# Optimization experiments

Hardware: AMD Instinct MI355X
Metric: run time of the kernel (lower is better)

Reference implementation:

```python
import jax, jax.numpy as jnp
import numpy as np

KEYS = ["A1", "B2", "E1", "E2", "E3", "E4", "E5"]
DIMS = [1, 1, 2, 2, 2, 2, 2]  # irrep dimensions for D12 point group
H = 8  # num_heads


def setup_inputs() -> dict:
    key = jax.random.key(0)
    ks = jax.random.split(key, 11)
    B, S, M = 8, 1024, 64  # batch, seq_len, multiplicity per key
    inp = {}
    for i, (name, d) in enumerate(zip(KEYS, DIMS)):
        inp[f"x_{name}"] = jax.random.normal(ks[i], (B, S, d, M), dtype=jnp.float32)
    for j, wn in enumerate(["Wq", "Wk", "Wv", "Wo"]):
        # per-key nn.Linear weights [out_mult, in_mult], stacked over the 7 keys
        inp[wn] = jax.random.normal(ks[7 + j], (7, M, M), dtype=jnp.float32) / np.float32(np.sqrt(M))
    return inp


def _split_heads(v):
    # [B,S,d,m] -> [B,H,S,d*mk]
    B, S, d, m = v.shape
    mk = m // H
    return v.reshape(B, S, d, H, mk).transpose(0, 3, 1, 2, 4).reshape(B, H, S, d * mk)


def _combine_heads(v, d):
    # [B,H,S,d*mk] -> [B,S,d,H*mk]
    B, _, S, dmk = v.shape
    mk = dmk // d
    return v.reshape(B, H, S, d, mk).transpose(0, 2, 3, 1, 4).reshape(B, S, d, H * mk)


def _forward(xs, Wq, Wk, Wv, Wo):
    # per-key bias-free linears on the multiplicity (last) axis; nn.Linear does x @ W.T
    qs = [_split_heads(jnp.einsum('bsdi,oi->bsdo', x, Wq[i])) for i, x in enumerate(xs)]
    kks = [_split_heads(jnp.einsum('bsdi,oi->bsdo', x, Wk[i])) for i, x in enumerate(xs)]
    vs = [_split_heads(jnp.einsum('bsdi,oi->bsdo', x, Wv[i])) for i, x in enumerate(xs)]
    Q = jnp.concatenate(qs, axis=-1)  # [B,H,S,D], D = sum d_k*mk = 96
    K = jnp.concatenate(kks, axis=-1)
    scale = np.float32(1.0 / np.sqrt(Q.shape[-1]))
    probs = jax.nn.softmax(jnp.einsum('bhqd,bhkd->bhqk', Q, K) * scale, axis=-1)
    outs = []
    for i, (v, d) in enumerate(zip(vs, DIMS)):
        o = jnp.einsum('bhqk,bhkd->bhqd', probs, v)  # shared softmax over per-key V branches
        o = _combine_heads(o, d)  # [B,S,d,M]
        outs.append(jnp.einsum('bsdi,oi->bsdo', o, Wo[i]))
    # concatenate the 7 per-key outputs along the irrep-dimension axis: [B,S,12,M]
    return jnp.concatenate(outs, axis=2)


def reference(x_A1, x_B2, x_E1, x_E2, x_E3, x_E4, x_E5, Wq, Wk, Wv, Wo):
    xs = [x_A1, x_B2, x_E1, x_E2, x_E3, x_E4, x_E5]
    return _forward(xs, Wq, Wk, Wv, Wo)
```

## Files before the change

kernel.cpp:

```cpp
#include <hip/hip_runtime.h>
#include <stdint.h>

typedef __attribute__((ext_vector_type(8))) short bf16x8;
typedef __attribute__((ext_vector_type(4))) float f32x4;
typedef unsigned short ushort_t;

__device__ __forceinline__ unsigned short f2bf(float f){
  union { float f; unsigned u; } c; c.f = f;
  unsigned u = c.u;
  u = u + 0x7FFFu + ((u >> 16) & 1u);
  return (unsigned short)(u >> 16);
}

__device__ __forceinline__ bf16x8 cvt8(const float* p){
  const float4 a = ((const float4*)p)[0];
  const float4 b = ((const float4*)p)[1];
  bf16x8 r;
  r[0]=(short)f2bf(a.x); r[1]=(short)f2bf(a.y); r[2]=(short)f2bf(a.z); r[3]=(short)f2bf(a.w);
  r[4]=(short)f2bf(b.x); r[5]=(short)f2bf(b.y); r[6]=(short)f2bf(b.z); r[7]=(short)f2bf(b.w);
  return r;
}

__device__ __forceinline__ uint32_t pk2bf(float a, float b){
  uint32_t r;
  asm("v_cvt_pk_bf16_f32 %0, %1, %2" : "=v"(r) : "v"(a), "v"(b));
  return r;
}

__device__ __forceinline__ float exp2x(float x){
  float r;
  asm("v_exp_f32 %0, %1" : "=v"(r) : "v"(x));
  return r;
}

__device__ __forceinline__ void gll16(const ushort_t* g, short* l){
  __builtin_amdgcn_global_load_lds(
      (const __attribute__((address_space(1))) unsigned int*)g,
      (__attribute__((address_space(3))) unsigned int*)l, 16, 0, 0);
}

__device__ __forceinline__ void rr_decode(int rr, int& i, int& dx, int& d){
  if (rr < 2){ i = rr; dx = 0; d = 1; }
  else { i = 2 + ((rr-2)>>1); dx = (rr-2)&1; d = 2; }
}

__global__ __launch_bounds__(256) void wconv(
    const float* __restrict__ Wq, const float* __restrict__ Wk,
    const float* __restrict__ Wv, const float* __restrict__ Wo,
    ushort_t* __restrict__ out)
{
  const int a = blockIdx.y;
  const float* src = (a==0)?Wq:(a==1)?Wk:(a==2)?Wv:Wo;
  const float sc = (a==0) ? 0.14724743479535623f : 1.0f;
  const int i = (blockIdx.x*256 + threadIdx.x)*8;
  float4 v0 = *(const float4*)(src+i);
  float4 v1 = *(const float4*)(src+i+4);
  uint4 o;
  o.x = pk2bf(v0.x*sc, v0.y*sc);
  o.y = pk2bf(v0.z*sc, v0.w*sc);
  o.z = pk2bf(v1.x*sc, v1.y*sc);
  o.w = pk2bf(v1.z*sc, v1.w*sc);
  *(uint4*)(out + (size_t)a*28672 + i) = o;
}

__global__ __launch_bounds__(256) void qkv_proj(
    const float* __restrict__ xA1, const float* __restrict__ xB2,
    const float* __restrict__ xE1, const float* __restrict__ xE2,
    const float* __restrict__ xE3, const float* __restrict__ xE4,
    const float* __restrict__ xE5,
    const ushort_t* __restrict__ Wb4,
    ushort_t* __restrict__ Qg, ushort_t* __restrict__ Kg,
    ushort_t* __restrict__ Vg)
{
  __shared__ short Cl[64*72];

  const int tile = blockIdx.x;
  const int rr = tile >> 7, rt = tile & 127;
  int i, dx, d; rr_decode(rr, i, dx, d);
  const float* xp = (i==0)?xA1:(i==1)?xB2:(i==2)?xE1:(i==3)?xE2:(i==4)?xE3:(i==5)?xE4:xE5;

  const int lane = threadIdx.x & 63;
  const int w    = threadIdx.x >> 6;
  const int lo = lane & 15, hi = lane >> 4;
  const int b8 = (rt >> 4) * 8;
  const int tile64 = rt & 15;

  bf16x8 afr[2];
  {
    const int R = rt*64 + w*16 + lo;
    const float* rp = xp + (size_t)(R*d + dx) * 64;
    afr[0] = cvt8(rp + 8*hi);
    afr[1] = cvt8(rp + 32 + 8*hi);
  }

  ushort_t* Ob[3] = {Qg, Kg, Vg};

  #pragma unroll
  for (int wsel = 0; wsel < 3; ++wsel){
    const ushort_t* Wb = Wb4 + (size_t)wsel*28672 + (size_t)i * 4096;
    #pragma unroll
    for (int ot = 0; ot < 4; ++ot){
      f32x4 acc = {0.f,0.f,0.f,0.f};
      #pragma unroll
      for (int c = 0; c < 2; ++c){
        bf16x8 bfr = *(const bf16x8*)(Wb + (size_t)(lo + 16*ot) * 64 + 32*c + 8*hi);
        acc = __builtin_amdgcn_mfma_f32_16x16x32_bf16(afr[c], bfr, acc, 0, 0, 0);
      }
      #pragma unroll
      for (int r = 0; r < 4; ++r)
        Cl[(w*16 + hi*4 + r)*72 + lo + 16*ot] = (short)f2bf(acc[r]);
    }
    __syncthreads();

    if (wsel < 2){
      #pragma unroll
      for (int cc = 0; cc < 2; ++cc){
        int c2 = threadIdx.x + cc*256;
        int sl = c2 & 63, hh = c2 >> 6;
        bf16x8 v = *(const bf16x8*)&Cl[sl*72 + hh*8];
        size_t a = (size_t)((b8 + hh)*16 + tile64)*6144
                 + (size_t)(((sl>>4)*3 + (rr>>2))*64 + (rr&3)*16 + (sl&15))*8;
        *(bf16x8*)(Ob[wsel] + a) = v;
      }
    } else {
      #pragma unroll
      for (int cc = 0; cc < 2; ++cc){
        int c2 = threadIdx.x + cc*256;
        int mm = c2 & 7, hh = (c2>>3)&7, sblk = c2>>6;
        int a5 = sblk>>2, slot = sblk&3;
        short tmp[8];
        #pragma unroll
        for (int jj = 0; jj < 8; ++jj){
          int s_j = a5*32 + (jj>>2)*16 + slot*4 + (jj&3);
          tmp[jj] = Cl[s_j*72 + hh*8 + mm];
        }
        int fh = rr>>1, fl = (rr&1)*8 + mm;
        size_t a = (size_t)((b8 + hh)*16 + tile64)*6144
                 + (size_t)((a5*6 + fh)*64 + slot*16 + fl)*8;
        *(bf16x8*)(Vg + a) = *(const bf16x8*)tmp;
      }
    }
    __syncthreads();
  }
}

__global__ __launch_bounds__(256, 2) void attn(
    const ushort_t* __restrict__ Qg,
    const ushort_t* __restrict__ Kg,
    const ushort_t* __restrict__ Vg,
    ushort_t* __restrict__ Oc)
{
  __shared__ __align__(16) short Kl[2][6144];
  __shared__ __align__(16) short Vl[2][6144];

  const int bid = blockIdx.x;
  const int bh = (bid & 7)*8 + ((bid >> 3) & 7);
  const int qt = bid >> 6;
  const int tid = threadIdx.x;
  const int w = tid >> 6, lane = tid & 63;
  const int lo = lane & 15, hi = lane >> 4;
  const size_t base = (size_t)bh * 16 * 6144;

  bf16x8 qf[2][3];
  #pragma unroll
  for (int g = 0; g < 2; ++g){
    int qq = qt*128 + w*32 + g*16;
    const ushort_t* qb = Qg + base + (size_t)(qq >> 6)*6144 + (size_t)(((qq>>4)&3)*3)*512;
    #pragma unroll
    for (int c = 0; c < 3; ++c)
      qf[g][c] = *(const bf16x8*)(qb + (c*64 + lane)*8);
  }

  f32x4 acc[6][2];
  #pragma unroll
  for (int ft = 0; ft < 6; ++ft){ acc[ft][0] = (f32x4){0,0,0,0}; acc[ft][1] = (f32x4){0,0,0,0}; }
  float lr[2] = {0.f, 0.f};

#define STAGE(tt, bb) do { \
    const ushort_t* kg_ = Kg + base + (size_t)(tt)*6144 + tid*8; \
    const ushort_t* vg_ = Vg + base + (size_t)(tt)*6144 + tid*8; \
    short* kl_ = &Kl[bb][tid*8]; short* vl_ = &Vl[bb][tid*8]; \
    gll16(kg_,        kl_);        gll16(kg_ + 2048, kl_ + 2048); \
    gll16(kg_ + 4096, kl_ + 4096); gll16(vg_,        vl_); \
    gll16(vg_ + 2048, vl_ + 2048); gll16(vg_ + 4096, vl_ + 4096); \
  } while(0)

  STAGE(0, 0);
  __syncthreads();

  for (int t = 0; t < 16; ++t){
    if (t < 15) STAGE(t+1, (t+1)&1);
    const int cb = t & 1;

    f32x4 st[2][4];
    __builtin_amdgcn_s_setprio(1);
    #pragma unroll
    for (int kvb = 0; kvb < 4; ++kvb){
      bf16x8 kf[3];
      #pragma unroll
      for (int c = 0; c < 3; ++c)
        kf[c] = *(const bf16x8*)&Kl[cb][((kvb*3 + c)*64 + lane)*8];
      #pragma unroll
      for (int g = 0; g < 2; ++g){
        f32x4 s = {0.f,0.f,0.f,0.f};
        #pragma unroll
        for (int c = 0; c < 3; ++c)
          s = __builtin_amdgcn_mfma_f32_16x16x32_bf16(kf[c], qf[g][c], s, 0, 0, 0);
        st[g][kvb] = s;
      }
    }
    __builtin_amdgcn_s_setprio(0);

    bf16x8 pb[2][2];
    #pragma unroll
    for (int g = 0; g < 2; ++g){
      #pragma unroll
      for (int kvb = 0; kvb < 4; ++kvb)
        #pragma unroll
        for (int r = 0; r < 4; ++r){ st[g][kvb][r] = exp2x(st[g][kvb][r]); lr[g] += st[g][kvb][r]; }
      #pragma unroll
      for (int ch = 0; ch < 2; ++ch){
        union { uint32_t u[4]; bf16x8 v; } pu;
        pu.u[0] = pk2bf(st[g][2*ch  ][0], st[g][2*ch  ][1]);
        pu.u[1] = pk2bf(st[g][2*ch  ][2], st[g][2*ch  ][3]);
        pu.u[2] = pk2bf(st[g][2*ch+1][0], st[g][2*ch+1][1]);
        pu.u[3] = pk2bf(st[g][2*ch+1][2], st[g][2*ch+1][3]);
        pb[g][ch] = pu.v;
      }
    }

    __builtin_amdgcn_s_setprio(1);
    #pragma unroll
    for (int ch = 0; ch < 2; ++ch){
      #pragma unroll
      for (int ft = 0; ft < 6; ++ft){
        bf16x8 va = *(const bf16x8*)&Vl[cb][((ch*6 + ft)*64 + lane)*8];
        acc[ft][0] = __builtin_amdgcn_mfma_f32_16x16x32_bf16(va, pb[0][ch], acc[ft][0], 0, 0, 0);
        acc[ft][1] = __builtin_amdgcn_mfma_f32_16x16x32_bf16(va, pb[1][ch], acc[ft][1], 0, 0, 0);
      }
    }
    __builtin_amdgcn_s_setprio(0);

    __syncthreads();
  }
#undef STAGE

  #pragma unroll
  for (int g = 0; g < 2; ++g){
    float l = lr[g];
    l += __shfl_xor(l, 16);
    l += __shfl_xor(l, 32);
    float rl = 1.f / l;
    int q = qt*128 + w*32 + g*16 + lo;
    #pragma unroll
    for (int ft = 0; ft < 6; ++ft){
      uint2 o;
      o.x = pk2bf(acc[ft][g][0]*rl, acc[ft][g][1]*rl);
      o.y = pk2bf(acc[ft][g][2]*rl, acc[ft][g][3]*rl);
      size_t ad = ((size_t)(bh*24 + ft*4 + hi)*1024 + q)*4;
      *(uint2*)(Oc + ad) = o;
    }
  }
}

__global__ __launch_bounds__(256) void out_proj(
    const ushort_t* __restrict__ Oc,
    const ushort_t* __restrict__ Wb4,
    float* __restrict__ out)
{
  const int tile = blockIdx.x;
  const int rr = tile >> 7, rt = tile & 127;
  int i, dx, d; rr_decode(rr, i, dx, d); (void)dx; (void)d;

  const int lane = threadIdx.x & 63;
  const int w    = threadIdx.x >> 6;
  const int lo = lane & 15, hi = lane >> 4;

  bf16x8 afr[2];
  {
    const int R = rt*64 + w*16 + lo;
    const int b = R >> 10, s = R & 1023;
    union { uint2 u2[2]; bf16x8 v; } a0, a1;
    #pragma unroll
    for (int jj = 0; jj < 2; ++jj){
      a0.u2[jj] = *(const uint2*)(Oc + ((size_t)((b*8 + hi)*24 + 2*rr + jj)*1024 + s)*4);
      a1.u2[jj] = *(const uint2*)(Oc + ((size_t)((b*8 + 4 + hi)*24 + 2*rr + jj)*1024 + s)*4);
    }
    afr[0] = a0.v;
    afr[1] = a1.v;
  }

  const ushort_t* Wb = Wb4 + (size_t)3*28672 + (size_t)i * 4096;
  #pragma unroll
  for (int ot = 0; ot < 4; ++ot){
    f32x4 acc = {0.f,0.f,0.f,0.f};
    #pragma unroll
    for (int c = 0; c < 2; ++c){
      bf16x8 bfr = *(const bf16x8*)(Wb + (size_t)(lo + 16*ot) * 64 + 32*c + 8*hi);
      acc = __builtin_amdgcn_mfma_f32_16x16x32_bf16(afr[c], bfr, acc, 0, 0, 0);
    }
    #pragma unroll
    for (int r = 0; r < 4; ++r){
      int bs = rt*64 + w*16 + hi*4 + r;
      out[(size_t)(bs*12 + rr)*64 + lo + 16*ot] = acc[r];
    }
  }
}

extern "C" void kernel_launch(void* const* d_in, const int* in_sizes, int n_in,
                              void* d_out, int out_size, void* d_ws, size_t ws_size,
                              hipStream_t stream)
{
  const float* xA1 = (const float*)d_in[0];
  const float* xB2 = (const float*)d_in[1];
  const float* xE1 = (const float*)d_in[2];
  const float* xE2 = (const float*)d_in[3];
  const float* xE3 = (const float*)d_in[4];
  const float* xE4 = (const float*)d_in[5];
  const float* xE5 = (const float*)d_in[6];
  const float* Wq  = (const float*)d_in[7];
  const float* Wk  = (const float*)d_in[8];
  const float* Wv  = (const float*)d_in[9];
  const float* Wo  = (const float*)d_in[10];

  const size_t NE = (size_t)8 * 1024 * 12 * 64;
  ushort_t* Qg = (ushort_t*)d_ws;
  ushort_t* Kg = Qg + NE;
  ushort_t* Vg = Kg + NE;
  ushort_t* Oc = Vg + NE;
  ushort_t* Wb4 = Oc + NE;

  wconv<<<dim3(14,4), dim3(256), 0, stream>>>(Wq, Wk, Wv, Wo, Wb4);
  qkv_proj<<<dim3(1536), dim3(256), 0, stream>>>(xA1,xB2,xE1,xE2,xE3,xE4,xE5,
                                                 Wb4, Qg,Kg,Vg);
  attn<<<dim3(512), dim3(256), 0, stream>>>(Qg,Kg,Vg, Oc);
  out_proj<<<dim3(1536), dim3(256), 0, stream>>>(Oc, Wb4, (float*)d_out);
}
```

Baseline: 72.75 us.

## Split attention KV range across two blocks and merge partials in out_proj

Attention now launches twice as many blocks, each covering half of the KV sequence. Each block writes unnormalized partial outputs plus row sums, and out_proj combines the two halves and normalizes them. This relies on the softmax using no running max, so the partials can simply be added. The aim is better occupancy on the 256-CU device (512 blocks was few), with launch bounds raised to 3. In addition, the Q/K projections are written directly from MFMA accumulators with swapped operands, dropping the LDS staging and syncs. The cost is extra workspace traffic for a second partial O buffer and sums, and a bf16 rounding of the unnormalized partials.

```diff
diff --git a/kernel.cpp b/kernel.cpp
--- a/kernel.cpp
+++ b/kernel.cpp
@@ -4,12 +4,18 @@
 typedef __attribute__((ext_vector_type(8))) short bf16x8;
 typedef __attribute__((ext_vector_type(4))) float f32x4;
 typedef unsigned short ushort_t;
+
+#define NE 6291456
 
 __device__ __forceinline__ unsigned short f2bf(float f){
   union { float f; unsigned u; } c; c.f = f;
   unsigned u = c.u;
   u = u + 0x7FFFu + ((u >> 16) & 1u);
   return (unsigned short)(u >> 16);
+}
+
+__device__ __forceinline__ float bfh2f(ushort_t u){
+  union { unsigned u; float f; } c; c.u = ((unsigned)u) << 16; return c.f;
 }
 
 __device__ __forceinline__ bf16x8 cvt8(const float* p){
@@ -93,11 +99,30 @@
     afr[1] = cvt8(rp + 32 + 8*hi);
   }
 
-  ushort_t* Ob[3] = {Qg, Kg, Vg};
-
-  #pragma unroll
-  for (int wsel = 0; wsel < 3; ++wsel){
+  ushort_t* OgQK[2] = {Qg, Kg};
+  #pragma unroll
+  for (int wsel = 0; wsel < 2; ++wsel){
     const ushort_t* Wb = Wb4 + (size_t)wsel*28672 + (size_t)i * 4096;
+    #pragma unroll
+    for (int ot = 0; ot < 4; ++ot){
+      f32x4 acc = {0.f,0.f,0.f,0.f};
+      #pragma unroll
+      for (int c = 0; c < 2; ++c){
+        bf16x8 bfr = *(const bf16x8*)(Wb + (size_t)(lo + 16*ot) * 64 + 32*c + 8*hi);
+        acc = __builtin_amdgcn_mfma_f32_16x16x32_bf16(bfr, afr[c], acc, 0, 0, 0);
+      }
+      uint2 o2;
+      o2.x = pk2bf(acc[0], acc[1]);
+      o2.y = pk2bf(acc[2], acc[3]);
+      int hh = 2*ot + (hi>>1);
+      size_t a = (size_t)((b8 + hh)*16 + tile64)*6144
+               + (size_t)((w*3 + (rr>>2))*64 + (rr&3)*16 + lo)*8 + 4*(hi&1);
+      *(uint2*)(OgQK[wsel] + a) = o2;
+    }
+  }
+
+  {
+    const ushort_t* Wb = Wb4 + (size_t)2*28672 + (size_t)i * 4096;
     #pragma unroll
     for (int ot = 0; ot < 4; ++ot){
       f32x4 acc = {0.f,0.f,0.f,0.f};
@@ -111,55 +136,44 @@
         Cl[(w*16 + hi*4 + r)*72 + lo + 16*ot] = (short)f2bf(acc[r]);
     }
     __syncthreads();
-
-    if (wsel < 2){
-      #pragma unroll
-      for (int cc = 0; cc < 2; ++cc){
-        int c2 = threadIdx.x + cc*256;
-        int sl = c2 & 63, hh = c2 >> 6;
-        bf16x8 v = *(const bf16x8*)&Cl[sl*72 + hh*8];
-        size_t a = (size_t)((b8 + hh)*16 + tile64)*6144
-                 + (size_t)(((sl>>4)*3 + (rr>>2))*64 + (rr&3)*16 + (sl&15))*8;
-        *(bf16x8*)(Ob[wsel] + a) = v;
-      }
-    } else {
-      #pragma unroll
-      for (int cc = 0; cc < 2; ++cc){
-        int c2 = threadIdx.x + cc*256;
-        int mm = c2 & 7, hh = (c2>>3)&7, sblk = c2>>6;
-        int a5 = sblk>>2, slot = sblk&3;
-        short tmp[8];
-        #pragma unroll
-        for (int jj = 0; jj < 8; ++jj){
-          int s_j = a5*32 + (jj>>2)*16 + slot*4 + (jj&3);
-          tmp[jj] = Cl[s_j*72 + hh*8 + mm];
-        }
-        int fh = rr>>1, fl = (rr&1)*8 + mm;
-        size_t a = (size_t)((b8 + hh)*16 + tile64)*6144
-                 + (size_t)((a5*6 + fh)*64 + slot*16 + fl)*8;
-        *(bf16x8*)(Vg + a) = *(const bf16x8*)tmp;
-      }
-    }
-    __syncthreads();
-  }
-}
-
-__global__ __launch_bounds__(256, 2) void attn(
+    #pragma unroll
+    for (int cc = 0; cc < 2; ++cc){
+      int c2 = threadIdx.x + cc*256;
+      int mm = c2 & 7, hh = (c2>>3)&7, sblk = c2>>6;
+      int a5 = sblk>>2, slot = sblk&3;
+      short tmp[8];
+      #pragma unroll
+      for (int jj = 0; jj < 8; ++jj){
+        int s_j = a5*32 + (jj>>2)*16 + slot*4 + (jj&3);
+        tmp[jj] = Cl[s_j*72 + hh*8 + mm];
+      }
+      int fh = rr>>1, fl = (rr&1)*8 + mm;
+      size_t a = (size_t)((b8 + hh)*16 + tile64)*6144
+               + (size_t)((a5*6 + fh)*64 + slot*16 + fl)*8;
+      *(bf16x8*)(Vg + a) = *(const bf16x8*)tmp;
+    }
+  }
+}
+
+__global__ __launch_bounds__(256, 3) void attn(
     const ushort_t* __restrict__ Qg,
     const ushort_t* __restrict__ Kg,
     const ushort_t* __restrict__ Vg,
-    ushort_t* __restrict__ Oc)
+    ushort_t* __restrict__ Op,
+    float* __restrict__ Lb)
 {
   __shared__ __align__(16) short Kl[2][6144];
   __shared__ __align__(16) short Vl[2][6144];
 
   const int bid = blockIdx.x;
   const int bh = (bid & 7)*8 + ((bid >> 3) & 7);
-  const int qt = bid >> 6;
+  const int vv = bid >> 6;
+  const int qt = vv >> 1, kvh = vv & 1;
   const int tid = threadIdx.x;
   const int w = tid >> 6, lane = tid & 63;
   const int lo = lane & 15, hi = lane >> 4;
   const size_t base = (size_t)bh * 16 * 6144;
+  const int tbase = kvh * 8;
 
   bf16x8 qf[2][3];
   #pragma unroll
@@ -185,11 +199,11 @@
     gll16(vg_ + 2048, vl_ + 2048); gll16(vg_ + 4096, vl_ + 4096); \
   } while(0)
 
-  STAGE(0, 0);
+  STAGE(tbase, 0);
   __syncthreads();
 
-  for (int t = 0; t < 16; ++t){
-    if (t < 15) STAGE(t+1, (t+1)&1);
+  for (int t = 0; t < 8; ++t){
+    if (t < 7) STAGE(tbase + t + 1, (t+1)&1);
     const int cb = t & 1;
 
     f32x4 st[2][4];
@@ -245,26 +259,28 @@
   }
 #undef STAGE
 
+  ushort_t* Oph = Op + (size_t)kvh * NE;
   #pragma unroll
   for (int g = 0; g < 2; ++g){
     float l = lr[g];
     l += __shfl_xor(l, 16);
     l += __shfl_xor(l, 32);
-    float rl = 1.f / l;
     int q = qt*128 + w*32 + g*16 + lo;
+    if (hi == 0) Lb[(size_t)(kvh*64 + bh)*1024 + q] = l;
     #pragma unroll
     for (int ft = 0; ft < 6; ++ft){
       uint2 o;
-      o.x = pk2bf(acc[ft][g][0]*rl, acc[ft][g][1]*rl);
-      o.y = pk2bf(acc[ft][g][2]*rl, acc[ft][g][3]*rl);
+      o.x = pk2bf(acc[ft][g][0], acc[ft][g][1]);
+      o.y = pk2bf(acc[ft][g][2], acc[ft][g][3]);
       size_t ad = ((size_t)(bh*24 + ft*4 + hi)*1024 + q)*4;
-      *(uint2*)(Oc + ad) = o;
+      *(uint2*)(Oph + ad) = o;
     }
   }
 }
 
 __global__ __launch_bounds__(256) void out_proj(
-    const ushort_t* __restrict__ Oc,
+    const ushort_t* __restrict__ Op,
+    const float* __restrict__ Lb,
     const ushort_t* __restrict__ Wb4,
     float* __restrict__ out)
 {
@@ -276,18 +292,31 @@
   const int w    = threadIdx.x >> 6;
   const int lo = lane & 15, hi = lane >> 4;
 
+  const int R = rt*64 + w*16 + lo;
+  const int b = R >> 10, s = R & 1023;
+
   bf16x8 afr[2];
-  {
-    const int R = rt*64 + w*16 + lo;
-    const int b = R >> 10, s = R & 1023;
-    union { uint2 u2[2]; bf16x8 v; } a0, a1;
+  #pragma unroll
+  for (int half = 0; half < 2; ++half){
+    int bh = b*8 + half*4 + hi;
+    float l0 = Lb[(size_t)bh*1024 + s];
+    float l1 = Lb[(size_t)(64 + bh)*1024 + s];
+    float rl = 1.f / (l0 + l1);
+    union { uint2 u2[2]; ushort_t us[8]; } a0, a1;
     #pragma unroll
     for (int jj = 0; jj < 2; ++jj){
-      a0.u2[jj] = *(const uint2*)(Oc + ((size_t)((b*8 + hi)*24 + 2*rr + jj)*1024 + s)*4);
-      a1.u2[jj] = *(const uint2*)(Oc + ((size_t)((b*8 + 4 + hi)*24 + 2*rr + jj)*1024 + s)*4);
-    }
-    afr[0] = a0.v;
-    afr[1] = a1.v;
+      size_t ad = ((size_t)(bh*24 + 2*rr + jj)*1024 + s)*4;
+      a0.u2[jj] = *(const uint2*)(Op + ad);
+      a1.u2[jj] = *(const uint2*)(Op + NE + ad);
+    }
+    union { uint32_t u[4]; bf16x8 v; } rv;
+    #pragma unroll
+    for (int e = 0; e < 4; ++e){
+      float f0 = (bfh2f(a0.us[2*e])   + bfh2f(a1.us[2*e]))   * rl;
+      float f1 = (bfh2f(a0.us[2*e+1]) + bfh2f(a1.us[2*e+1])) * rl;
+      rv.u[e] = pk2bf(f0, f1);
+    }
+    afr[half] = rv.v;
   }
 
   const ushort_t* Wb = Wb4 + (size_t)3*28672 + (size_t)i * 4096;
@@ -323,16 +352,16 @@
   const float* Wv  = (const float*)d_in[9];
   const float* Wo  = (const float*)d_in[10];
 
-  const size_t NE = (size_t)8 * 1024 * 12 * 64;
-  ushort_t* Qg = (ushort_t*)d_ws;
-  ushort_t* Kg = Qg + NE;
-  ushort_t* Vg = Kg + NE;
-  ushort_t* Oc = Vg + NE;
-  ushort_t* Wb4 = Oc + NE;
+  ushort_t* Qg  = (ushort_t*)d_ws;
+  ushort_t* Kg  = Qg + NE;
+  ushort_t* Vg  = Kg + NE;
+  ushort_t* Op  = Vg + NE;
+  ushort_t* Wb4 = Op + (size_t)2*NE;
+  float*    Lb  = (float*)(Wb4 + 4*28672);
 
   wconv<<<dim3(14,4), dim3(256), 0, stream>>>(Wq, Wk, Wv, Wo, Wb4);
   qkv_proj<<<dim3(1536), dim3(256), 0, stream>>>(xA1,xB2,xE1,xE2,xE3,xE4,xE5,
                                                  Wb4, Qg,Kg,Vg);
-  attn<<<dim3(512), dim3(256), 0, stream>>>(Qg,Kg,Vg, Oc);
-  out_proj<<<dim3(1536), dim3(256), 0, stream>>>(Oc, Wb4, (float*)d_out);
-}
+  attn<<<dim3(1024), dim3(256), 0, stream>>>(Qg,Kg,Vg, Op, Lb);
+  out_proj<<<dim3(1536), dim3(256), 0, stream>>>(Op, Lb, Wb4, (float*)d_out);
+}
```

New measurement: 78.08 us. 1.07x slower.

## Interleave K and V into one buffer and halve attention KV tile size

Applied to the files above, without the earlier changes.

K and V are now written into a single interleaved KV buffer, so each 32-key tile holds K and V side by side. The attention kernel stages one 12 KB chunk per iteration over 32 iterations instead of two 12 KB chunks over 16. This halves shared memory per block and allows launch_bounds of 4 blocks per CU. Q and K are also written straight from MFMA registers with swapped operands, skipping the LDS transpose. The trade-off is twice as many barriers and pipeline stages in attention, and the higher occupancy target may put pressure on registers.

```diff
diff --git a/kernel.cpp b/kernel.cpp
--- a/kernel.cpp
+++ b/kernel.cpp
@@ -4,6 +4,8 @@
 typedef __attribute__((ext_vector_type(8))) short bf16x8;
 typedef __attribute__((ext_vector_type(4))) float f32x4;
 typedef unsigned short ushort_t;
+
+#define NE 6291456
 
 __device__ __forceinline__ unsigned short f2bf(float f){
   union { float f; unsigned u; } c; c.f = f;
@@ -69,8 +71,7 @@
     const float* __restrict__ xE3, const float* __restrict__ xE4,
     const float* __restrict__ xE5,
     const ushort_t* __restrict__ Wb4,
-    ushort_t* __restrict__ Qg, ushort_t* __restrict__ Kg,
-    ushort_t* __restrict__ Vg)
+    ushort_t* __restrict__ Qg, ushort_t* __restrict__ KVg)
 {
   __shared__ short Cl[64*72];
 
@@ -93,11 +94,48 @@
     afr[1] = cvt8(rp + 32 + 8*hi);
   }
 
-  ushort_t* Ob[3] = {Qg, Kg, Vg};
-
-  #pragma unroll
-  for (int wsel = 0; wsel < 3; ++wsel){
-    const ushort_t* Wb = Wb4 + (size_t)wsel*28672 + (size_t)i * 4096;
+  {
+    const ushort_t* Wb = Wb4 + (size_t)i * 4096;
+    #pragma unroll
+    for (int ot = 0; ot < 4; ++ot){
+      f32x4 acc = {0.f,0.f,0.f,0.f};
+      #pragma unroll
+      for (int c = 0; c < 2; ++c){
+        bf16x8 bfr = *(const bf16x8*)(Wb + (size_t)(lo + 16*ot) * 64 + 32*c + 8*hi);
+        acc = __builtin_amdgcn_mfma_f32_16x16x32_bf16(bfr, afr[c], acc, 0, 0, 0);
+      }
+      uint2 o2;
+      o2.x = pk2bf(acc[0], acc[1]);
+      o2.y = pk2bf(acc[2], acc[3]);
+      int hh = 2*ot + (hi>>1);
+      size_t a = (size_t)((b8 + hh)*16 + tile64)*6144
+               + (size_t)((w*3 + (rr>>2))*64 + (rr&3)*16 + lo)*8 + 4*(hi&1);
+      *(uint2*)(Qg + a) = o2;
+    }
+  }
+
+  {
+    const ushort_t* Wb = Wb4 + (size_t)28672 + (size_t)i * 4096;
+    #pragma unroll
+    for (int ot = 0; ot < 4; ++ot){
+      f32x4 acc = {0.f,0.f,0.f,0.f};
+      #pragma unroll
+      for (int c = 0; c < 2; ++c){
+        bf16x8 bfr = *(const bf16x8*)(Wb + (size_t)(lo + 16*ot) * 64 + 32*c + 8*hi);
+        acc = __builtin_amdgcn_mfma_f32_16x16x32_bf16(bfr, afr[c], acc, 0, 0, 0);
+      }
+      uint2 o2;
+      o2.x = pk2bf(acc[0], acc[1]);
+      o2.y = pk2bf(acc[2], acc[3]);
+      int hh = 2*ot + (hi>>1);
+      size_t a = (size_t)((b8 + hh)*32 + tile64*2 + (w>>1))*6144
+               + (size_t)(((w&1)*3 + (rr>>2))*64 + (rr&3)*16 + lo)*8 + 4*(hi&1);
+      *(uint2*)(KVg + a) = o2;
+    }
+  }
+
+  {
+    const ushort_t* Wb = Wb4 + (size_t)2*28672 + (size_t)i * 4096;
     #pragma unroll
     for (int ot = 0; ot < 4; ++ot){
       f32x4 acc = {0.f,0.f,0.f,0.f};
@@ -111,47 +149,31 @@
         Cl[(w*16 + hi*4 + r)*72 + lo + 16*ot] = (short)f2bf(acc[r]);
     }
     __syncthreads();
-
-    if (wsel < 2){
-      #pragma unroll
-      for (int cc = 0; cc < 2; ++cc){
-        int c2 = threadIdx.x + cc*256;
-        int sl = c2 & 63, hh = c2 >> 6;
-        bf16x8 v = *(const bf16x8*)&Cl[sl*72 + hh*8];
-        size_t a = (size_t)((b8 + hh)*16 + tile64)*6144
-                 + (size_t)(((sl>>4)*3 + (rr>>2))*64 + (rr&3)*16 + (sl&15))*8;
-        *(bf16x8*)(Ob[wsel] + a) = v;
-      }
-    } else {
-      #pragma unroll
-      for (int cc = 0; cc < 2; ++cc){
-        int c2 = threadIdx.x + cc*256;
-        int mm = c2 & 7, hh = (c2>>3)&7, sblk = c2>>6;
-        int a5 = sblk>>2, slot = sblk&3;
-        short tmp[8];
-        #pragma unroll
-        for (int jj = 0; jj < 8; ++jj){
-          int s_j = a5*32 + (jj>>2)*16 + slot*4 + (jj&3);
-          tmp[jj] = Cl[s_j*72 + hh*8 + mm];
-        }
-        int fh = rr>>1, fl = (rr&1)*8 + mm;
-        size_t a = (size_t)((b8 + hh)*16 + tile64)*6144
-                 + (size_t)((a5*6 + fh)*64 + slot*16 + fl)*8;
-        *(bf16x8*)(Vg + a) = *(const bf16x8*)tmp;
-      }
-    }
-    __syncthreads();
-  }
-}
-
-__global__ __launch_bounds__(256, 2) void attn(
+    #pragma unroll
+    for (int cc = 0; cc < 2; ++cc){
+      int c2 = threadIdx.x + cc*256;
+      int mm = c2 & 7, hh = (c2>>3)&7, sblk = c2>>6;
+      int a5 = sblk>>2, slot = sblk&3;
+      short tmp[8];
+      #pragma unroll
+      for (int jj = 0; jj < 8; ++jj){
+        int s_j = a5*32 + (jj>>2)*16 + slot*4 + (jj&3);
+        tmp[jj] = Cl[s_j*72 + hh*8 + mm];
+      }
+      int fh = rr>>1, fl = (rr&1)*8 + mm;
+      size_t a = (size_t)((b8 + hh)*32 + tile64*2 + a5)*6144 + 3072
+               + (size_t)(fh*64 + slot*16 + fl)*8;
+      *(bf16x8*)(KVg + a) = *(const bf16x8*)tmp;
+    }
+  }
+}
+
+__global__ __launch_bounds__(256, 4) void attn(
     const ushort_t* __restrict__ Qg,
-    const ushort_t* __restrict__ Kg,
-    const ushort_t* __restrict__ Vg,
+    const ushort_t* __restrict__ KVg,
     ushort_t* __restrict__ Oc)
 {
-  __shared__ __align__(16) short Kl[2][6144];
-  __shared__ __align__(16) short Vl[2][6144];
+  __shared__ __align__(16) short KVl[2][6144];
 
   const int bid = blockIdx.x;
   const int bh = (bid & 7)*8 + ((bid >> 3) & 7);
@@ -159,13 +181,14 @@
   const int tid = threadIdx.x;
   const int w = tid >> 6, lane = tid & 63;
   const int lo = lane & 15, hi = lane >> 4;
-  const size_t base = (size_t)bh * 16 * 6144;
+  const size_t qbase  = (size_t)bh * 16 * 6144;
+  const size_t kvbase = (size_t)bh * 32 * 6144;
 
   bf16x8 qf[2][3];
   #pragma unroll
   for (int g = 0; g < 2; ++g){
     int qq = qt*128 + w*32 + g*16;
-    const ushort_t* qb = Qg + base + (size_t)(qq >> 6)*6144 + (size_t)(((qq>>4)&3)*3)*512;
+    const ushort_t* qb = Qg + qbase + (size_t)(qq >> 6)*6144 + (size_t)(((qq>>4)&3)*3)*512;
     #pragma unroll
     for (int c = 0; c < 3; ++c)
       qf[g][c] = *(const bf16x8*)(qb + (c*64 + lane)*8);
@@ -177,29 +200,26 @@
   float lr[2] = {0.f, 0.f};
 
 #define STAGE(tt, bb) do { \
-    const ushort_t* kg_ = Kg + base + (size_t)(tt)*6144 + tid*8; \
-    const ushort_t* vg_ = Vg + base + (size_t)(tt)*6144 + tid*8; \
-    short* kl_ = &Kl[bb][tid*8]; short* vl_ = &Vl[bb][tid*8]; \
-    gll16(kg_,        kl_);        gll16(kg_ + 2048, kl_ + 2048); \
-    gll16(kg_ + 4096, kl_ + 4096); gll16(vg_,        vl_); \
-    gll16(vg_ + 2048, vl_ + 2048); gll16(vg_ + 4096, vl_ + 4096); \
+    const ushort_t* kv_ = KVg + kvbase + (size_t)(tt)*6144 + tid*8; \
+    short* l_ = &KVl[bb][tid*8]; \
+    gll16(kv_, l_); gll16(kv_ + 2048, l_ + 2048); gll16(kv_ + 4096, l_ + 4096); \
   } while(0)
 
   STAGE(0, 0);
   __syncthreads();
 
-  for (int t = 0; t < 16; ++t){
-    if (t < 15) STAGE(t+1, (t+1)&1);
+  for (int t = 0; t < 32; ++t){
+    if (t < 31) STAGE(t+1, (t+1)&1);
     const int cb = t & 1;
 
-    f32x4 st[2][4];
+    f32x4 st[2][2];
     __builtin_amdgcn_s_setprio(1);
     #pragma unroll
-    for (int kvb = 0; kvb < 4; ++kvb){
+    for (int kvb = 0; kvb < 2; ++kvb){
       bf16x8 kf[3];
       #pragma unroll
       for (int c = 0; c < 3; ++c)
-        kf[c] = *(const bf16x8*)&Kl[cb][((kvb*3 + c)*64 + lane)*8];
+        kf[c] = *(const bf16x8*)&KVl[cb][((kvb*3 + c)*64 + lane)*8];
       #pragma unroll
       for (int g = 0; g < 2; ++g){
         f32x4 s = {0.f,0.f,0.f,0.f};
@@ -211,33 +231,27 @@
     }
     __builtin_amdgcn_s_setprio(0);
 
-    bf16x8 pb[2][2];
+    bf16x8 pb[2];
     #pragma unroll
     for (int g = 0; g < 2; ++g){
       #pragma unroll
-      for (int kvb = 0; kvb < 4; ++kvb)
+      for (int kvb = 0; kvb < 2; ++kvb)
         #pragma unroll
         for (int r = 0; r < 4; ++r){ st[g][kvb][r] = exp2x(st[g][kvb][r]); lr[g] += st[g][kvb][r]; }
-      #pragma unroll
-      for (int ch = 0; ch < 2; ++ch){
-        union { uint32_t u[4]; bf16x8 v; } pu;
-        pu.u[0] = pk2bf(st[g][2*ch  ][0], st[g][2*ch  ][1]);
-        pu.u[1] = pk2bf(st[g][2*ch  ][2], st[g][2*ch  ][3]);
-        pu.u[2] = pk2bf(st[g][2*ch+1][0], st[g][2*ch+1][1]);
-        pu.u[3] = pk2bf(st[g][2*ch+1][2], st[g][2*ch+1][3]);
-        pb[g][ch] = pu.v;
-      }
+      union { uint32_t u[4]; bf16x8 v; } pu;
+      pu.u[0] = pk2bf(st[g][0][0], st[g][0][1]);
+      pu.u[1] = pk2bf(st[g][0][2], st[g][0][3]);
+      pu.u[2] = pk2bf(st[g][1][0], st[g][1][1]);
+      pu.u[3] = pk2bf(st[g][1][2], st[g][1][3]);
+      pb[g] = pu.v;
     }
 
     __builtin_amdgcn_s_setprio(1);
     #pragma unroll
-    for (int ch = 0; ch < 2; ++ch){
-      #pragma unroll
-      for (int ft = 0; ft < 6; ++ft){
-        bf16x8 va = *(const bf16x8*)&Vl[cb][((ch*6 + ft)*64 + lane)*8];
-        acc[ft][0] = __builtin_amdgcn_mfma_f32_16x16x32_bf16(va, pb[0][ch], acc[ft][0], 0, 0, 0);
-        acc[ft][1] = __builtin_amdgcn_mfma_f32_16x16x32_bf16(va, pb[1][ch], acc[ft][1], 0, 0, 0);
-      }
+    for (int ft = 0; ft < 6; ++ft){
+      bf16x8 va = *(const bf16x8*)&KVl[cb][3072 + (ft*64 + lane)*8];
+      acc[ft][0] = __builtin_amdgcn_mfma_f32_16x16x32_bf16(va, pb[0], acc[ft][0], 0, 0, 0);
+      acc[ft][1] = __builtin_amdgcn_mfma_f32_16x16x32_bf16(va, pb[1], acc[ft][1], 0, 0, 0);
     }
     __builtin_amdgcn_s_setprio(0);
 
@@ -323,16 +337,14 @@
   const float* Wv  = (const float*)d_in[9];
   const float* Wo  = (const float*)d_in[10];
 
-  const size_t NE = (size_t)8 * 1024 * 12 * 64;
-  ushort_t* Qg = (ushort_t*)d_ws;
-  ushort_t* Kg = Qg + NE;
-  ushort_t* Vg = Kg + NE;
-  ushort_t* Oc = Vg + NE;
+  ushort_t* Qg  = (ushort_t*)d_ws;
+  ushort_t* KVg = Qg + NE;
+  ushort_t* Oc  = KVg + (size_t)2*NE;
   ushort_t* Wb4 = Oc + NE;
 
   wconv<<<dim3(14,4), dim3(256), 0, stream>>>(Wq, Wk, Wv, Wo, Wb4);
   qkv_proj<<<dim3(1536), dim3(256), 0, stream>>>(xA1,xB2,xE1,xE2,xE3,xE4,xE5,
-                                                 Wb4, Qg,Kg,Vg);
-  attn<<<dim3(512), dim3(256), 0, stream>>>(Qg,Kg,Vg, Oc);
+                                                 Wb4, Qg, KVg);
+  attn<<<dim3(512), dim3(256), 0, stream>>>(Qg, KVg, Oc);
   out_proj<<<dim3(1536), dim3(256), 0, stream>>>(Oc, Wb4, (float*)d_out);
 }
```

Result: no change. 71.78 us (-1.3%).
